# Optimization experiments

Measured on AMD Instinct MI355X. Metric: run time of the kernel, lower is better.

Reference implementation:

```python
import jax, jax.numpy as jnp
import numpy as np

DIST = 7
ROUNDS = 25
A = DIST ** 2 - 1              # n_ancillas = 48
ND = A * (A + 1) // 2          # 1176 upper-triangular entries


def _triangular_polmap():
    diag, nondiag = [], []
    for iy in range(A):
        for ix in range(iy, A):
            if ix != iy:
                nondiag.append(ix + iy * A)
            else:
                diag.append(ix + iy * A)
    return np.asarray(diag + nondiag, dtype=np.int32)

POLMAP = jnp.asarray(_triangular_polmap())  # (ND,)


def setup_inputs() -> dict:
    key = jax.random.key(0)
    k1, k2, k3 = jax.random.split(key, 3)
    x = jax.random.randint(k1, (4096, ROUNDS, A), 0, 2, dtype=jnp.int32)
    emb_diag = jax.random.normal(k2, (1, A), dtype=jnp.float32)
    emb_nondiag = jax.random.normal(k3, (1, ND - A, 4), dtype=jnp.float32)
    return {"x": x, "emb_diag": emb_diag, "emb_nondiag": emb_nondiag}


def reference(x, emb_diag, emb_nondiag):
    B, R, _ = x.shape
    # transformed embedding params (shared across rounds / batch via broadcast)
    sig_diag = jax.nn.sigmoid(emb_diag)                       # (1, A)
    f12 = jax.nn.sigmoid(emb_nondiag[:, :, 0])
    f9 = jax.nn.sigmoid(emb_nondiag[:, :, 1]) * f12
    f8 = jax.nn.sigmoid(emb_nondiag[:, :, 2]) * f9
    f6 = jax.nn.sigmoid(emb_nondiag[:, :, 3]) * f8
    fnd = jnp.stack([f12, f9, f8, f6], axis=2)                # (1, ND-A, 4)

    # sliding windows of 3 consecutive rounds, round axis leading for scan
    a = jnp.moveaxis(x[:, 0:R - 2, :], 1, 0)                  # (R-2, B, A)
    b = jnp.moveaxis(x[:, 1:R - 1, :], 1, 0)
    c = jnp.moveaxis(x[:, 2:R, :], 1, 0)

    def step(carry, abc):
        st, dt = carry                                         # int32 (B, A)
        ai, bi, ci = abc
        data_err = ai + ci - ai * ci * 2
        meas_err = bi * (1 - (ai + ci)) + ai * ci
        dt = dt * (1 - meas_err * 2)
        st = jnp.clip(st + dt * data_err, -1, 1)
        dt = dt * (1 - st * st * (1 - meas_err)) - st * (1 - meas_err)
        # quadratic (outer-product) state, values in {4,6,8,9,12,16}
        xx = st + 3
        outer = (xx[:, :, None] * xx[:, None, :]).reshape(B, A * A)
        tri = jnp.take(outer, POLMAP, axis=1)                  # (B, ND)
        rd, rn = tri[:, :A], tri[:, A:]
        diag_val = (rd == 16).astype(jnp.float32) + (rd == 9).astype(jnp.float32) * sig_diag
        nmask = jnp.stack([rn == 12, rn == 9, rn == 8, rn == 6], axis=2).astype(jnp.float32)
        nd_val = (rn == 16).astype(jnp.float32) + jnp.sum(nmask * fnd, axis=2)
        out = jnp.concatenate([diag_val, nd_val], axis=1)      # (B, ND)
        return (st, dt), out

    st0 = -jnp.ones((B, A), jnp.int32)
    dt0 = jnp.ones((B, A), jnp.int32)
    _, ys = jax.lax.scan(step, (st0, dt0), (a, b, c))          # (R-2, B, ND)
    return jnp.moveaxis(ys, 0, 1)                              # (B, R-2, ND)
```

## Files before the change

### kernel.cpp

```cpp
#include <hip/hip_runtime.h>
#include <math.h>

#define AA 48
#define RR 25
#define TT 23
#define ND 1176
#define NOFF 1128
#define NT 320
#define NOWN 294

typedef float vfloat4 __attribute__((ext_vector_type(4)));

#define GTAB_BYTES (ND * 16)

__global__ __launch_bounds__(256) void build_tables_kernel(
    const float* __restrict__ emb_diag,
    const float* __restrict__ emb_nd,
    float4* __restrict__ gtab,
    uint32_t* __restrict__ pairs)
{
    int p = blockIdx.x * 256 + threadIdx.x;
    if (p >= ND) return;
    if (p < AA) {
        pairs[p] = (uint32_t)(p | (p << 8));
        float s = 1.0f / (1.0f + __expf(-emb_diag[p]));
        gtab[p] = make_float4(0.0f, s, 0.0f, 0.0f);
    } else {
        int pp = p - AA;
        int iy = (int)((95.0f - sqrtf(9025.0f - 8.0f * (float)pp)) * 0.5f);
        if (iy < 0) iy = 0;
        if (iy > 46) iy = 46;
        while (iy < 46 && (47 * (iy + 1) - ((iy + 1) * iy) / 2) <= pp) ++iy;
        while (iy > 0 && (47 * iy - (iy * (iy - 1)) / 2) > pp) --iy;
        int S  = 47 * iy - (iy * (iy - 1)) / 2;
        int ix = iy + 1 + (pp - S);
        pairs[p] = (uint32_t)(iy | (ix << 8));
        const float* e = emb_nd + pp * 4;
        float f12 = 1.0f / (1.0f + __expf(-e[0]));
        float f9  = f12 / (1.0f + __expf(-e[1]));
        float f8  = f9  / (1.0f + __expf(-e[2]));
        float f6  = f8  / (1.0f + __expf(-e[3]));
        gtab[p] = make_float4(f12, f9, f8, f6);
    }
}

__global__ __launch_bounds__(NT) void cnn_embed_kernel(
    const int*      __restrict__ x,
    const float4*   __restrict__ gtab,
    const uint32_t* __restrict__ pairs,
    float*          __restrict__ out,
    int B)
{
    __shared__ uint8_t xls[RR * AA];
    __shared__ uint8_t xxc[TT * AA];

    const int tid = threadIdx.x;
    const int b   = blockIdx.x;
    if (b >= B) return;

    const bool owner = (tid < NOWN);
    int iidx[4], jidx[4];
    float4 g[4];
    if (owner) {
        uint4 pr = ((const uint4*)pairs)[tid];
        iidx[0] = pr.x & 0xFF; jidx[0] = (pr.x >> 8) & 0xFF;
        iidx[1] = pr.y & 0xFF; jidx[1] = (pr.y >> 8) & 0xFF;
        iidx[2] = pr.z & 0xFF; jidx[2] = (pr.z >> 8) & 0xFF;
        iidx[3] = pr.w & 0xFF; jidx[3] = (pr.w >> 8) & 0xFF;
        #pragma unroll
        for (int k = 0; k < 4; ++k) g[k] = gtab[4 * tid + k];
    }

    {
        const int4* xg = (const int4*)(x + (size_t)b * RR * AA);
        if (tid < (RR * AA) / 4) {
            int4 v = xg[tid];
            uint32_t packed = (uint32_t)(v.x & 1) | ((uint32_t)(v.y & 1) << 8) |
                              ((uint32_t)(v.z & 1) << 16) | ((uint32_t)(v.w & 1) << 24);
            *((uint32_t*)&xls[tid * 4]) = packed;
        }
    }
    __syncthreads();

    if (tid < AA) {
        const int j = tid;
        int st = -1, dt = 1;
        #pragma unroll
        for (int t = 0; t < TT; ++t) {
            int a  = xls[t * AA + j];
            int bv = xls[(t + 1) * AA + j];
            int c  = xls[(t + 2) * AA + j];
            int de = a ^ c;
            int me = de ? 0 : (a ^ bv);
            if (me) dt = -dt;
            st += dt * de;
            st = st < -1 ? -1 : (st > 1 ? 1 : st);
            if (!me) dt = (st == 0) ? dt : -st;
            xxc[t * AA + j] = (uint8_t)(st + 3);
        }
    }
    __syncthreads();

    if (owner) {
        float* ob = out + (size_t)b * TT * ND + tid * 4;
        for (int t = 0; t < TT; ++t) {
            const uint8_t* xr = &xxc[t * AA];
            vfloat4 v;
            #pragma unroll
            for (int k = 0; k < 4; ++k) {
                int prod = (int)xr[iidx[k]] * (int)xr[jidx[k]];
                float r = 0.0f;
                r = (prod == 6)  ? g[k].w : r;
                r = (prod == 8)  ? g[k].z : r;
                r = (prod == 9)  ? g[k].y : r;
                r = (prod == 12) ? g[k].x : r;
                r = (prod == 16) ? 1.0f   : r;
                v[k] = r;
            }
            __builtin_nontemporal_store(v, (vfloat4*)(ob + (size_t)t * ND));
        }
    }
}

extern "C" void kernel_launch(void* const* d_in, const int* in_sizes, int n_in,
                              void* d_out, int out_size, void* d_ws, size_t ws_size,
                              hipStream_t stream) {
    const int*   x  = (const int*)d_in[0];
    const float* ed = (const float*)d_in[1];
    const float* en = (const float*)d_in[2];
    float* out = (float*)d_out;
    float4*   gtab  = (float4*)d_ws;
    uint32_t* pairs = (uint32_t*)((char*)d_ws + GTAB_BYTES);
    const int B = in_sizes[0] / (RR * AA);

    hipLaunchKernelGGL(build_tables_kernel, dim3((ND + 255) / 256), dim3(256), 0, stream,
                       ed, en, gtab, pairs);
    hipLaunchKernelGGL(cnn_embed_kernel, dim3(B), dim3(NT), 0, stream,
                       x, gtab, pairs, out, B);
}
```

Baseline: 486.1 us.

## Split recurrence into separate kernel and stream embedding over time chunks

Moves the per-ancilla sign recurrence into its own kernel that writes compact uint8 states to workspace, one thread per (batch, ancilla). A second kernel then splits each batch's 23 rounds into 4 chunks per block, so there are four times as many blocks and each does a shorter store loop. Nontemporal stores are replaced with plain float4 stores. The cost is an extra launch, a workspace round trip, and reloading the pair and gtab tables in every chunk block; the fused kernel is kept as a fallback when the workspace is too small.

After: 475.3 us. -2.2%, faster.

```diff
diff --git a/kernel.cpp b/kernel.cpp
--- a/kernel.cpp
+++ b/kernel.cpp
@@ -5,13 +5,14 @@
 #define RR 25
 #define TT 23
 #define ND 1176
-#define NOFF 1128
 #define NT 320
 #define NOWN 294
-
-typedef float vfloat4 __attribute__((ext_vector_type(4)));
+#define XXB (TT * AA)
+#define TCH 6
+#define CHUNKS 4
 
 #define GTAB_BYTES (ND * 16)
+#define TABLES_BYTES (GTAB_BYTES + ND * 4)
 
 __global__ __launch_bounds__(256) void build_tables_kernel(
     const float* __restrict__ emb_diag,
@@ -44,6 +45,90 @@
     }
 }
 
+__global__ __launch_bounds__(256) void rec_kernel(
+    const int* __restrict__ x,
+    uint8_t*   __restrict__ xx,
+    int B)
+{
+    int idx = blockIdx.x * 256 + threadIdx.x;
+    if (idx >= B * AA) return;
+    int b = idx / AA;
+    int j = idx - b * AA;
+    const int* xb = x + (size_t)b * RR * AA + j;
+    uint8_t*   o  = xx + (size_t)b * XXB + j;
+    int st = -1, dt = 1;
+    int a  = xb[0] & 1;
+    int bv = xb[AA] & 1;
+    #pragma unroll
+    for (int t = 0; t < TT; ++t) {
+        int c  = xb[(t + 2) * AA] & 1;
+        int de = a ^ c;
+        int me = de ? 0 : (a ^ bv);
+        if (me) dt = -dt;
+        st += dt * de;
+        st = st < -1 ? -1 : (st > 1 ? 1 : st);
+        if (!me) dt = (st == 0) ? dt : -st;
+        o[t * AA] = (uint8_t)(st + 3);
+        a = bv; bv = c;
+    }
+}
+
+__global__ __launch_bounds__(NT) void embed_stream_kernel(
+    const uint8_t*  __restrict__ xx,
+    const float4*   __restrict__ gtab,
+    const uint32_t* __restrict__ pairs,
+    float*          __restrict__ out,
+    int B)
+{
+    __shared__ uint8_t row[TCH * AA];
+    const int blk = blockIdx.x;
+    const int b   = blk >> 2;
+    const int ch  = blk & 3;
+    const int t0  = ch * TCH;
+    int nt = TT - t0; if (nt > TCH) nt = TCH;
+    const int tid = threadIdx.x;
+
+    if (tid < nt * (AA / 4)) {
+        const uint32_t* src = (const uint32_t*)(xx + (size_t)b * XXB + t0 * AA);
+        ((uint32_t*)row)[tid] = src[tid];
+    }
+
+    const bool owner = (tid < NOWN);
+    int iidx[4], jidx[4];
+    float4 g[4];
+    if (owner) {
+        uint4 pr = ((const uint4*)pairs)[tid];
+        iidx[0] = pr.x & 0xFF; jidx[0] = (pr.x >> 8) & 0xFF;
+        iidx[1] = pr.y & 0xFF; jidx[1] = (pr.y >> 8) & 0xFF;
+        iidx[2] = pr.z & 0xFF; jidx[2] = (pr.z >> 8) & 0xFF;
+        iidx[3] = pr.w & 0xFF; jidx[3] = (pr.w >> 8) & 0xFF;
+        #pragma unroll
+        for (int k = 0; k < 4; ++k) g[k] = gtab[4 * tid + k];
+    }
+    __syncthreads();
+
+    if (owner) {
+        float* ob = out + ((size_t)b * TT + t0) * ND + tid * 4;
+        for (int tt = 0; tt < nt; ++tt) {
+            const uint8_t* xr = &row[tt * AA];
+            float4 v;
+            float* vf = (float*)&v;
+            #pragma unroll
+            for (int k = 0; k < 4; ++k) {
+                int prod = (int)xr[iidx[k]] * (int)xr[jidx[k]];
+                float r = 0.0f;
+                r = (prod == 6)  ? g[k].w : r;
+                r = (prod == 8)  ? g[k].z : r;
+                r = (prod == 9)  ? g[k].y : r;
+                r = (prod == 12) ? g[k].x : r;
+                r = (prod == 16) ? 1.0f   : r;
+                vf[k] = r;
+            }
+            *((float4*)(ob + (size_t)tt * ND)) = v;
+        }
+    }
+}
+
 __global__ __launch_bounds__(NT) void cnn_embed_kernel(
     const int*      __restrict__ x,
     const float4*   __restrict__ gtab,
@@ -105,7 +190,8 @@
         float* ob = out + (size_t)b * TT * ND + tid * 4;
         for (int t = 0; t < TT; ++t) {
             const uint8_t* xr = &xxc[t * AA];
-            vfloat4 v;
+            float4 v;
+            float* vf = (float*)&v;
             #pragma unroll
             for (int k = 0; k < 4; ++k) {
                 int prod = (int)xr[iidx[k]] * (int)xr[jidx[k]];
@@ -115,9 +201,9 @@
                 r = (prod == 9)  ? g[k].y : r;
                 r = (prod == 12) ? g[k].x : r;
                 r = (prod == 16) ? 1.0f   : r;
-                v[k] = r;
+                vf[k] = r;
             }
-            __builtin_nontemporal_store(v, (vfloat4*)(ob + (size_t)t * ND));
+            *((float4*)(ob + (size_t)t * ND)) = v;
         }
     }
 }
@@ -131,10 +217,21 @@
     float* out = (float*)d_out;
     float4*   gtab  = (float4*)d_ws;
     uint32_t* pairs = (uint32_t*)((char*)d_ws + GTAB_BYTES);
+    uint8_t*  xx    = (uint8_t*)((char*)d_ws + TABLES_BYTES);
     const int B = in_sizes[0] / (RR * AA);
 
     hipLaunchKernelGGL(build_tables_kernel, dim3((ND + 255) / 256), dim3(256), 0, stream,
                        ed, en, gtab, pairs);
-    hipLaunchKernelGGL(cnn_embed_kernel, dim3(B), dim3(NT), 0, stream,
-                       x, gtab, pairs, out, B);
-}
+
+    const size_t need = (size_t)TABLES_BYTES + (size_t)B * XXB;
+    if (ws_size >= need) {
+        const int rthreads = B * AA;
+        hipLaunchKernelGGL(rec_kernel, dim3((rthreads + 255) / 256), dim3(256), 0, stream,
+                           x, xx, B);
+        hipLaunchKernelGGL(embed_stream_kernel, dim3(B * CHUNKS), dim3(NT), 0, stream,
+                           xx, gtab, pairs, out, B);
+    } else {
+        hipLaunchKernelGGL(cnn_embed_kernel, dim3(B), dim3(NT), 0, stream,
+                           x, gtab, pairs, out, B);
+    }
+}
```
